# Kernel tuning notes

Hardware: AMD Instinct MI355X
Metric: run time of the kernel (lower is better)

## Reference

```python
import jax, jax.numpy as jnp
import numpy as np

N_NODES = 100_000
N_EDGES = 20_000   # hyperedges
NNZ = 2_000_000    # incidence pairs
F = 128
BN_EPS = 1e-5


def setup_inputs() -> dict:
    key = jax.random.key(0)
    ks = jax.random.split(key, 6)
    x_0 = jax.random.normal(ks[0], (N_NODES, F), dtype=jnp.float32)
    x_1 = jax.random.normal(ks[1], (N_EDGES, F), dtype=jnp.float32)
    node_idx = jax.random.randint(ks[2], (NNZ,), 0, N_NODES, dtype=jnp.int32)
    edge_idx = jax.random.randint(ks[3], (NNZ,), 0, N_EDGES, dtype=jnp.int32)
    W_nh = jax.random.normal(ks[4], (F, F), dtype=jnp.float32) / np.float32(np.sqrt(F))
    b_nh = jnp.zeros((F,), jnp.float32)
    W_en = jax.random.normal(ks[5], (F, 2 * F), dtype=jnp.float32) / np.float32(np.sqrt(2 * F))
    b_en = jnp.zeros((F,), jnp.float32)
    ones = jnp.ones((F,), jnp.float32)
    zeros = jnp.zeros((F,), jnp.float32)
    return {
        "x_0": x_0, "x_1": x_1, "node_idx": node_idx, "edge_idx": edge_idx,
        "W_nh": W_nh, "b_nh": b_nh, "W_en": W_en, "b_en": b_en,
        "bn0_gamma": ones, "bn0_beta": zeros, "bn0_mean": zeros, "bn0_var": ones,
        "bn1_gamma": ones, "bn1_beta": zeros, "bn1_mean": zeros, "bn1_var": ones,
    }


def _bn_eval(x, gamma, beta, mean, var):
    # BatchNorm1d in eval mode: normalize with running stats.
    return (x - mean) * (gamma * jax.lax.rsqrt(var + BN_EPS)) + beta


def reference(x_0, x_1, node_idx, edge_idx, W_nh, b_nh, W_en, b_en,
              bn0_gamma, bn0_beta, bn0_mean, bn0_var,
              bn1_gamma, bn1_beta, bn1_mean, bn1_var):
    # --- node -> hyperedge messenger ---
    # per-node message: sigmoid(Linear(x_0))  [n_nodes, F]
    node_messages = jax.nn.sigmoid(x_0 @ W_nh.T + b_nh)
    # gather over incidence list, scatter-sum onto hyperedges  [n_edges, F]
    node_msg_agg = jax.ops.segment_sum(node_messages[node_idx], edge_idx,
                                       num_segments=N_EDGES)

    # --- hyperedge -> node messenger ---
    # per-hyperedge message: sigmoid(Linear(cat(x_1, agg node msgs)))  [n_edges, F]
    he_messages = jax.nn.sigmoid(
        jnp.concatenate([x_1, node_msg_agg], axis=1) @ W_en.T + b_en)
    # gather per incidence, scatter-sum onto nodes  [n_nodes, F]
    he_msg_agg = jax.ops.segment_sum(he_messages[edge_idx], node_idx,
                                     num_segments=N_NODES)

    # --- updates (eval mode: feature dropout is identity) ---
    x0_out = jax.nn.sigmoid(
        _bn_eval(x_0, bn0_gamma, bn0_beta, bn0_mean, bn0_var) + he_msg_agg)
    x1_out = jax.nn.sigmoid(
        _bn_eval(x_1, bn1_gamma, bn1_beta, bn1_mean, bn1_var) + node_msg_agg)
    return (x0_out, x1_out)
```

## Files before the change

### kernel.cpp

```cpp
#include <hip/hip_runtime.h>
#include <hip/hip_bf16.h>
#include <math.h>

#define NNODES 100000
#define NEDGES 20000
#define NNZ_   2000000
#define FDIM   128
#define BN_EPS 1e-5f

#define NBUCK 256
#define CAP   9216
#define BPB_E 79
#define BPB_N 391
#define SH_E  17
#define SH_N  15

typedef __attribute__((ext_vector_type(8))) short bf16x8_t;
typedef __attribute__((ext_vector_type(4))) float f32x4_t;
typedef __attribute__((ext_vector_type(8))) unsigned short u16x8_t;

__device__ __forceinline__ float sigmoidf_(float x) {
    return 1.0f / (1.0f + __expf(-x));
}
__device__ __forceinline__ float bf2f(unsigned short u) {
    return __uint_as_float(((unsigned)u) << 16);
}
__device__ __forceinline__ unsigned short f2bf(float f) {
    __hip_bfloat16 h = __float2bfloat16(f);
    return *reinterpret_cast<unsigned short*>(&h);
}

__global__ __launch_bounds__(256) void prep_w(
    const float* __restrict__ W_nh, const float* __restrict__ W_en,
    unsigned short* __restrict__ Wnh_bf, float* __restrict__ WTen)
{
    int idx = blockIdx.x * blockDim.x + threadIdx.x;
    if (idx < FDIM * FDIM) {
        Wnh_bf[idx] = f2bf(W_nh[idx]);
    } else {
        int j = idx - FDIM * FDIM;
        if (j >= 2 * FDIM * FDIM) return;
        int k = j >> 7, c = j & 127;
        WTen[j] = W_en[c * 2 * FDIM + k];
    }
}

__global__ __launch_bounds__(256) void gemm1_mfma(
    const float* __restrict__ x0, const unsigned short* __restrict__ Wb,
    const float* __restrict__ bias, unsigned short* __restrict__ out)
{
    __shared__ unsigned short As[32][FDIM + 8];
    const int tid  = threadIdx.x;
    const int row0 = blockIdx.x * 32;
    {
        int r = tid >> 3, c0 = (tid & 7) * 16;
        const float* src = x0 + (size_t)(row0 + r) * FDIM + c0;
        unsigned short* dst = &As[r][c0];
        #pragma unroll
        for (int i = 0; i < 4; i++) {
            float4 v = *(const float4*)(src + i * 4);
            dst[i * 4 + 0] = f2bf(v.x);
            dst[i * 4 + 1] = f2bf(v.y);
            dst[i * 4 + 2] = f2bf(v.z);
            dst[i * 4 + 3] = f2bf(v.w);
        }
    }
    __syncthreads();
    const int wave  = tid >> 6;
    const int lane  = tid & 63;
    const int mhalf = wave & 1;
    const int nhalf = wave >> 1;
    const int lm    = lane & 15;
    const int quad  = lane >> 4;
    f32x4_t acc[4] = {};
    #pragma unroll
    for (int ks = 0; ks < 4; ks++) {
        bf16x8_t a = *(const bf16x8_t*)&As[mhalf * 16 + lm][ks * 32 + quad * 8];
        #pragma unroll
        for (int nt = 0; nt < 4; nt++) {
            int n = nhalf * 64 + nt * 16 + lm;
            bf16x8_t b = *(const bf16x8_t*)(Wb + (size_t)n * FDIM + ks * 32 + quad * 8);
            acc[nt] = __builtin_amdgcn_mfma_f32_16x16x32_bf16(a, b, acc[nt], 0, 0, 0);
        }
    }
    const int mbase = row0 + mhalf * 16 + quad * 4;
    #pragma unroll
    for (int nt = 0; nt < 4; nt++) {
        int n = nhalf * 64 + nt * 16 + lm;
        float bv = bias[n];
        #pragma unroll
        for (int r2 = 0; r2 < 4; r2++) {
            out[(size_t)(mbase + r2) * FDIM + n] = f2bf(sigmoidf_(acc[nt][r2] + bv));
        }
    }
}

__global__ __launch_bounds__(256, 2) void gemm_sig_bf16(
    const float* __restrict__ A1, const float* __restrict__ A2,
    const float* __restrict__ WT, const float* __restrict__ bias,
    unsigned short* __restrict__ out)
{
    constexpr int K = 256, BK = 64;
    __shared__ float As[32][BK + 4];
    __shared__ float Ws[BK][FDIM];
    const int tid  = threadIdx.x;
    const int row0 = blockIdx.x * 32;
    const int tcol = tid & 31;
    const int trow = tid >> 5;
    float acc[4][4] = {};
    for (int kk = 0; kk < K; kk += BK) {
        const float* Asrc = (kk < FDIM) ? A1 : A2;
        const int koff    = (kk < FDIM) ? kk : kk - FDIM;
        #pragma unroll
        for (int i = 0; i < 2; i++) {
            int l = tid + i * 256;
            int r = l >> 4, j = l & 15;
            float4 v = *(const float4*)(Asrc + (size_t)(row0 + r) * FDIM + koff + j * 4);
            *(float4*)&As[r][j * 4] = v;
        }
        #pragma unroll
        for (int i = 0; i < 8; i++) {
            int l = tid + i * 256;
            int k = l >> 5, j = l & 31;
            float4 v = *(const float4*)(WT + (size_t)(kk + k) * FDIM + j * 4);
            *(float4*)&Ws[k][j * 4] = v;
        }
        __syncthreads();
        #pragma unroll
        for (int k = 0; k < BK; k += 4) {
            float4 a[4];
            #pragma unroll
            for (int r = 0; r < 4; r++)
                a[r] = *(const float4*)&As[trow * 4 + r][k];
            #pragma unroll
            for (int kq = 0; kq < 4; kq++) {
                float4 w = *(const float4*)&Ws[k + kq][tcol * 4];
                #pragma unroll
                for (int r = 0; r < 4; r++) {
                    float av = (kq == 0) ? a[r].x : (kq == 1) ? a[r].y
                             : (kq == 2) ? a[r].z : a[r].w;
                    acc[r][0] += av * w.x;
                    acc[r][1] += av * w.y;
                    acc[r][2] += av * w.z;
                    acc[r][3] += av * w.w;
                }
            }
        }
        __syncthreads();
    }
    float4 bv = *(const float4*)(bias + tcol * 4);
    #pragma unroll
    for (int r = 0; r < 4; r++) {
        int row = row0 + trow * 4 + r;
        ushort4 o;
        o.x = f2bf(sigmoidf_(acc[r][0] + bv.x));
        o.y = f2bf(sigmoidf_(acc[r][1] + bv.y));
        o.z = f2bf(sigmoidf_(acc[r][2] + bv.z));
        o.w = f2bf(sigmoidf_(acc[r][3] + bv.w));
        *(ushort4*)(out + (size_t)row * FDIM + tcol * 4) = o;
    }
}

__global__ __launch_bounds__(1024) void bucket_scatter(
    const int* __restrict__ ni, const int* __restrict__ ei,
    unsigned* __restrict__ buck_e, unsigned* __restrict__ buck_n,
    int* __restrict__ gcur_e, int* __restrict__ gcur_n)
{
    __shared__ int lh_e[NBUCK], lh_n[NBUCK], lb_e[NBUCK], lb_n[NBUCK];
    const int t = threadIdx.x;
    if (t < NBUCK) { lh_e[t] = 0; lh_n[t] = 0; }
    __syncthreads();
    unsigned ent_e[4], ent_n[4];
    int be[4], bn[4], re[4], rn[4];
    const int base = blockIdx.x * 4096;
    #pragma unroll
    for (int j = 0; j < 4; j++) {
        int i = base + j * 1024 + t;
        if (i < NNZ_) {
            unsigned n = (unsigned)ni[i], e = (unsigned)ei[i];
            ent_e[j] = (e << SH_E) | n;  be[j] = (int)(e / BPB_E);
            ent_n[j] = (n << SH_N) | e;  bn[j] = (int)(n / BPB_N);
            re[j] = atomicAdd(&lh_e[be[j]], 1);
            rn[j] = atomicAdd(&lh_n[bn[j]], 1);
        } else { be[j] = -1; }
    }
    __syncthreads();
    if (t < NBUCK) {
        lb_e[t] = t * CAP + atomicAdd(&gcur_e[t], lh_e[t]);
        lb_n[t] = t * CAP + atomicAdd(&gcur_n[t], lh_n[t]);
    }
    __syncthreads();
    #pragma unroll
    for (int j = 0; j < 4; j++) {
        if (be[j] >= 0) {
            buck_e[(size_t)lb_e[be[j]] + re[j]] = ent_e[j];
            buck_n[(size_t)lb_n[bn[j]] + rn[j]] = ent_n[j];
        }
    }
}

template<int BPB, int SH, unsigned MASK, int NBINS, typename OUT>
__device__ __forceinline__ void sort_bucket(
    const unsigned* __restrict__ region, int cnt, int gbase, int b0,
    OUT* __restrict__ csr, int* __restrict__ off)
{
    __shared__ unsigned lh[512];
    __shared__ unsigned lw[4];
    const int t = threadIdx.x;
    lh[t] = 0; lh[t + 256] = 0;
    __syncthreads();
    for (int i = t; i < cnt; i += 256) {
        int bin = (int)(region[i] >> SH) - b0;
        atomicAdd(&lh[bin], 1u);
    }
    __syncthreads();
    unsigned h0 = lh[2 * t], h1 = lh[2 * t + 1];
    unsigned s = h0 + h1, inc = s;
    const int lane = t & 63;
    #pragma unroll
    for (int d = 1; d <= 32; d <<= 1) {
        unsigned v = (unsigned)__shfl_up((int)inc, d, 64);
        if (lane >= d) inc += v;
    }
    if (lane == 63) lw[t >> 6] = inc;
    __syncthreads();
    unsigned pre = 0;
    #pragma unroll
    for (int w = 0; w < 4; w++) if (w < (t >> 6)) pre += lw[w];
    unsigned excl = pre + inc - s;
    unsigned c0 = (unsigned)gbase + excl;
    unsigned c1 = c0 + h0;
    lh[2 * t] = c0; lh[2 * t + 1] = c1;
    int i0 = 2 * t, i1 = 2 * t + 1;
    if (i0 <= BPB && b0 + i0 <= NBINS) off[b0 + i0] = (int)c0;
    if (i1 <= BPB && b0 + i1 <= NBINS) off[b0 + i1] = (int)c1;
    __syncthreads();
    for (int i = t; i < cnt; i += 256) {
        unsigned ent = region[i];
        int bin = (int)(ent >> SH) - b0;
        unsigned pos = atomicAdd(&lh[bin], 1u);
        csr[pos] = (OUT)(ent & MASK);
    }
}

__global__ __launch_bounds__(256) void bucket_sort(
    const unsigned* __restrict__ buck_e, const unsigned* __restrict__ buck_n,
    const int* __restrict__ gcur_e, const int* __restrict__ gcur_n,
    unsigned* __restrict__ csr_e, unsigned short* __restrict__ csr_n,
    int* __restrict__ off_e, int* __restrict__ off_n)
{
    const int b = blockIdx.x & 255;
    const int* gc = (blockIdx.x < 256) ? gcur_e : gcur_n;
    __shared__ int ws4[4];
    const int t = threadIdx.x;
    int v = (t < b) ? gc[t] : 0;
    #pragma unroll
    for (int d = 32; d > 0; d >>= 1) v += __shfl_down(v, d, 64);
    if ((t & 63) == 0) ws4[t >> 6] = v;
    __syncthreads();
    const int gbase = ws4[0] + ws4[1] + ws4[2] + ws4[3];
    const int cnt = gc[b];
    __syncthreads();
    if (blockIdx.x < 256)
        sort_bucket<BPB_E, SH_E, 0x1FFFFu, NEDGES, unsigned>(
            buck_e + (size_t)b * CAP, cnt, gbase, b * BPB_E, csr_e, off_e);
    else
        sort_bucket<BPB_N, SH_N, 0x7FFFu, NNODES, unsigned short>(
            buck_n + (size_t)b * CAP, cnt, gbase, b * BPB_N, csr_n, off_n);
}

template<typename IDX, int U>
__global__ __launch_bounds__(256) void seg_sum_fin_v2(
    const unsigned short* __restrict__ table, const IDX* __restrict__ csr,
    const int* __restrict__ off, const float* __restrict__ x,
    const float* __restrict__ g, const float* __restrict__ bb,
    const float* __restrict__ mm, const float* __restrict__ vv,
    float* __restrict__ agg_out, float* __restrict__ fin_out, int nseg)
{
    const int seg = blockIdx.x * 4 + (threadIdx.x >> 6);
    if (seg >= nseg) return;
    const int lane = threadIdx.x & 63;
    const int c    = lane & 15;
    const int sub  = lane >> 4;
    const int c8   = c * 8;

    const int i0 = off[seg], i1 = off[seg + 1];
    f32x4_t a0 = {}, a1 = {};

    int i = i0;
    for (; i + 4 * U <= i1; i += 4 * U) {
        int r[U];
        u16x8_t v[U];
        #pragma unroll
        for (int u = 0; u < U; u++) r[u] = (int)csr[i + 4 * u + sub];
        #pragma unroll
        for (int u = 0; u < U; u++)
            v[u] = *(const u16x8_t*)(table + (size_t)r[u] * FDIM + c8);
        #pragma unroll
        for (int u = 0; u < U; u++) {
            a0[0] += bf2f(v[u][0]); a0[1] += bf2f(v[u][1]);
            a0[2] += bf2f(v[u][2]); a0[3] += bf2f(v[u][3]);
            a1[0] += bf2f(v[u][4]); a1[1] += bf2f(v[u][5]);
            a1[2] += bf2f(v[u][6]); a1[3] += bf2f(v[u][7]);
        }
    }
    if (i < i1) {
        u16x8_t v[U];
        #pragma unroll
        for (int u = 0; u < U; u++) {
            int row = i + 4 * u + sub;
            u16x8_t z = 0;
            v[u] = z;
            if (row < i1)
                v[u] = *(const u16x8_t*)(table + (size_t)csr[row] * FDIM + c8);
        }
        #pragma unroll
        for (int u = 0; u < U; u++) {
            a0[0] += bf2f(v[u][0]); a0[1] += bf2f(v[u][1]);
            a0[2] += bf2f(v[u][2]); a0[3] += bf2f(v[u][3]);
            a1[0] += bf2f(v[u][4]); a1[1] += bf2f(v[u][5]);
            a1[2] += bf2f(v[u][6]); a1[3] += bf2f(v[u][7]);
        }
    }

    #pragma unroll
    for (int j = 0; j < 4; j++) {
        a0[j] += __shfl_xor(a0[j], 16, 64);
        a0[j] += __shfl_xor(a0[j], 32, 64);
        a1[j] += __shfl_xor(a1[j], 16, 64);
        a1[j] += __shfl_xor(a1[j], 32, 64);
    }

    if (sub < 2) {
        const int q = c8 + sub * 4;
        f32x4_t s = sub ? a1 : a0;
        if (agg_out)
            *(f32x4_t*)(agg_out + (size_t)seg * FDIM + q) = s;
        if (fin_out) {
            f32x4_t xv = *(const f32x4_t*)(x + (size_t)seg * FDIM + q);
            f32x4_t gg = *(const f32x4_t*)(g + q);
            f32x4_t bt = *(const f32x4_t*)(bb + q);
            f32x4_t mn = *(const f32x4_t*)(mm + q);
            f32x4_t vr = *(const f32x4_t*)(vv + q);
            f32x4_t o;
            #pragma unroll
            for (int j = 0; j < 4; j++)
                o[j] = sigmoidf_((xv[j] - mn[j]) * (gg[j] * rsqrtf(vr[j] + BN_EPS))
                                 + bt[j] + s[j]);
            *(f32x4_t*)(fin_out + (size_t)seg * FDIM + q) = o;
        }
    }
}

extern "C" void kernel_launch(void* const* d_in, const int* in_sizes, int n_in,
                              void* d_out, int out_size, void* d_ws, size_t ws_size,
                              hipStream_t stream)
{
    const float* x0       = (const float*)d_in[0];
    const float* x1       = (const float*)d_in[1];
    const int*   node_idx = (const int*)d_in[2];
    const int*   edge_idx = (const int*)d_in[3];
    const float* W_nh     = (const float*)d_in[4];
    const float* b_nh     = (const float*)d_in[5];
    const float* W_en     = (const float*)d_in[6];
    const float* b_en     = (const float*)d_in[7];
    const float* bn0g = (const float*)d_in[8];
    const float* bn0b = (const float*)d_in[9];
    const float* bn0m = (const float*)d_in[10];
    const float* bn0v = (const float*)d_in[11];
    const float* bn1g = (const float*)d_in[12];
    const float* bn1b = (const float*)d_in[13];
    const float* bn1m = (const float*)d_in[14];
    const float* bn1v = (const float*)d_in[15];

    float* ws = (float*)d_ws;
    float* B    = ws;
    float* WTen = B + (size_t)NEDGES * FDIM;
    unsigned short* Wnh_bf = (unsigned short*)(WTen + 2 * FDIM * FDIM);
    unsigned short* A_bf = Wnh_bf + FDIM * FDIM;
    unsigned short* D_bf = A_bf + (size_t)NNODES * FDIM;
    int* ip    = (int*)(D_bf + (size_t)NEDGES * FDIM);
    int* off_e = ip;
    int* off_n = off_e + 20004;
    unsigned* csr_e = (unsigned*)(off_n + 100004);
    unsigned short* csr_n = (unsigned short*)(csr_e + NNZ_);
    unsigned* buck_e = (unsigned*)(csr_n + NNZ_);
    unsigned* buck_n = buck_e + (size_t)NBUCK * CAP;
    int* gcur_e = (int*)(buck_n + (size_t)NBUCK * CAP);
    int* gcur_n = gcur_e + NBUCK;

    hipMemsetAsync(gcur_e, 0, 2 * NBUCK * sizeof(int), stream);
    bucket_scatter<<<(NNZ_ + 4095) / 4096, 1024, 0, stream>>>(
        node_idx, edge_idx, buck_e, buck_n, gcur_e, gcur_n);
    bucket_sort<<<2 * NBUCK, 256, 0, stream>>>(buck_e, buck_n, gcur_e, gcur_n,
                                               csr_e, csr_n, off_e, off_n);

    prep_w<<<(3 * FDIM * FDIM + 255) / 256, 256, 0, stream>>>(W_nh, W_en, Wnh_bf, WTen);

    float* out0 = (float*)d_out;
    float* out1 = out0 + (size_t)NNODES * FDIM;

    gemm1_mfma<<<NNODES / 32, 256, 0, stream>>>(x0, Wnh_bf, b_nh, A_bf);
    seg_sum_fin_v2<unsigned, 8><<<(NEDGES + 3) / 4, 256, 0, stream>>>(
        A_bf, csr_e, off_e, x1, bn1g, bn1b, bn1m, bn1v, B, out1, NEDGES);

    gemm_sig_bf16<<<NEDGES / 32, 256, 0, stream>>>(x1, B, WTen, b_en, D_bf);
    seg_sum_fin_v2<unsigned short, 4><<<(NNODES + 3) / 4, 256, 0, stream>>>(
        D_bf, csr_n, off_n, x0, bn0g, bn0b, bn0m, bn0v, nullptr, out0, NNODES);
}
```

Baseline: 389.9 us.

## Split node-to-edge gather into node-range partitions and fuse reduction into GEMM2

The edge-side CSR is sorted by (edge, node-slice), giving 8 partitions per hyperedge. A new kernel gathers each partition separately into fp32 partial buffers, which spreads the gather across 8x more blocks and keeps each block's table reads within one node slice for better cache locality. A fused GEMM then sums the partials, writes the x1 output with batch norm and sigmoid, and computes the edge messages. This adds partial-buffer traffic and a larger offset array, and it needs enough workspace; if there is not enough, a fallback path is used.

```diff
diff --git a/kernel.cpp b/kernel.cpp
--- a/kernel.cpp
+++ b/kernel.cpp
@@ -14,6 +14,8 @@
 #define BPB_N 391
 #define SH_E  17
 #define SH_N  15
+#define NPART 8
+#define PSLICE 12500
 
 typedef __attribute__((ext_vector_type(8))) short bf16x8_t;
 typedef __attribute__((ext_vector_type(4))) float f32x4_t;
@@ -161,6 +163,99 @@
     }
 }
 
+__global__ __launch_bounds__(256, 2) void gemm2_fused(
+    const float* __restrict__ A1, const float* __restrict__ part,
+    const float* __restrict__ WT, const float* __restrict__ bias,
+    const float* __restrict__ g1, const float* __restrict__ b1,
+    const float* __restrict__ m1, const float* __restrict__ v1,
+    float* __restrict__ out1, unsigned short* __restrict__ outD)
+{
+    constexpr int K = 256, BK = 64;
+    __shared__ float As[32][BK + 4];
+    __shared__ float Ws[BK][FDIM];
+    const int tid  = threadIdx.x;
+    const int row0 = blockIdx.x * 32;
+    const int tcol = tid & 31;
+    const int trow = tid >> 5;
+    float acc[4][4] = {};
+    for (int kk = 0; kk < K; kk += BK) {
+        if (kk < FDIM) {
+            #pragma unroll
+            for (int i = 0; i < 2; i++) {
+                int l = tid + i * 256;
+                int r = l >> 4, j = l & 15;
+                float4 v = *(const float4*)(A1 + (size_t)(row0 + r) * FDIM + kk + j * 4);
+                *(float4*)&As[r][j * 4] = v;
+            }
+        } else {
+            const int koff = kk - FDIM;
+            #pragma unroll
+            for (int i = 0; i < 2; i++) {
+                int l = tid + i * 256;
+                int r = l >> 4, j = l & 15;
+                int col = koff + j * 4;
+                const float* pp = part + (size_t)(row0 + r) * FDIM + col;
+                f32x4_t bsum = {};
+                #pragma unroll
+                for (int p = 0; p < NPART; p++)
+                    bsum += *(const f32x4_t*)(pp + (size_t)p * NEDGES * FDIM);
+                *(f32x4_t*)&As[r][j * 4] = bsum;
+                f32x4_t xv = *(const f32x4_t*)(A1 + (size_t)(row0 + r) * FDIM + col);
+                f32x4_t gg = *(const f32x4_t*)(g1 + col);
+                f32x4_t bt = *(const f32x4_t*)(b1 + col);
+                f32x4_t mn = *(const f32x4_t*)(m1 + col);
+                f32x4_t vr = *(const f32x4_t*)(v1 + col);
+                f32x4_t o;
+                #pragma unroll
+                for (int jj = 0; jj < 4; jj++)
+                    o[jj] = sigmoidf_((xv[jj] - mn[jj]) * (gg[jj] * rsqrtf(vr[jj] + BN_EPS))
+                                      + bt[jj] + bsum[jj]);
+                *(f32x4_t*)(out1 + (size_t)(row0 + r) * FDIM + col) = o;
+            }
+        }
+        #pragma unroll
+        for (int i = 0; i < 8; i++) {
+            int l = tid + i * 256;
+            int k = l >> 5, j = l & 31;
+            float4 v = *(const float4*)(WT + (size_t)(kk + k) * FDIM + j * 4);
+            *(float4*)&Ws[k][j * 4] = v;
+        }
+        __syncthreads();
+        #pragma unroll
+        for (int k = 0; k < BK; k += 4) {
+            float4 a[4];
+            #pragma unroll
+            for (int r = 0; r < 4; r++)
+                a[r] = *(const float4*)&As[trow * 4 + r][k];
+            #pragma unroll
+            for (int kq = 0; kq < 4; kq++) {
+                float4 w = *(const float4*)&Ws[k + kq][tcol * 4];
+                #pragma unroll
+                for (int r = 0; r < 4; r++) {
+                    float av = (kq == 0) ? a[r].x : (kq == 1) ? a[r].y
+                             : (kq == 2) ? a[r].z : a[r].w;
+                    acc[r][0] += av * w.x;
+                    acc[r][1] += av * w.y;
+                    acc[r][2] += av * w.z;
+                    acc[r][3] += av * w.w;
+                }
+            }
+        }
+        __syncthreads();
+    }
+    float4 bv = *(const float4*)(bias + tcol * 4);
+    #pragma unroll
+    for (int r = 0; r < 4; r++) {
+        int row = row0 + trow * 4 + r;
+        ushort4 o;
+        o.x = f2bf(sigmoidf_(acc[r][0] + bv.x));
+        o.y = f2bf(sigmoidf_(acc[r][1] + bv.y));
+        o.z = f2bf(sigmoidf_(acc[r][2] + bv.z));
+        o.w = f2bf(sigmoidf_(acc[r][3] + bv.w));
+        *(ushort4*)(outD + (size_t)row * FDIM + tcol * 4) = o;
+    }
+}
+
 __global__ __launch_bounds__(1024) void bucket_scatter(
     const int* __restrict__ ni, const int* __restrict__ ei,
     unsigned* __restrict__ buck_e, unsigned* __restrict__ buck_n,
@@ -199,10 +294,58 @@
     }
 }
 
-template<int BPB, int SH, unsigned MASK, int NBINS, typename OUT>
-__device__ __forceinline__ void sort_bucket(
+__device__ __forceinline__ int ep_bin(unsigned ent) {
+    int e = (int)(ent >> SH_E);
+    int n = (int)(ent & 0x1FFFFu);
+    return e * NPART + n / PSLICE;
+}
+
+__device__ __forceinline__ void sort_bucket_e(
+    const unsigned* __restrict__ region, int cnt, int gbase, int bucket,
+    unsigned* __restrict__ csr, int* __restrict__ off)
+{
+    __shared__ unsigned lh[768];
+    __shared__ unsigned lw[4];
+    const int t = threadIdx.x;
+    lh[t] = 0; lh[t + 256] = 0; lh[t + 512] = 0;
+    __syncthreads();
+    const int b0 = bucket * (BPB_E * NPART);
+    for (int i = t; i < cnt; i += 256)
+        atomicAdd(&lh[ep_bin(region[i]) - b0], 1u);
+    __syncthreads();
+    unsigned h0 = lh[3 * t], h1 = lh[3 * t + 1], h2 = lh[3 * t + 2];
+    unsigned s = h0 + h1 + h2, inc = s;
+    const int lane = t & 63;
+    #pragma unroll
+    for (int d = 1; d <= 32; d <<= 1) {
+        unsigned v = (unsigned)__shfl_up((int)inc, d, 64);
+        if (lane >= d) inc += v;
+    }
+    if (lane == 63) lw[t >> 6] = inc;
+    __syncthreads();
+    unsigned pre = 0;
+    #pragma unroll
+    for (int w = 0; w < 4; w++) if (w < (t >> 6)) pre += lw[w];
+    unsigned excl = pre + inc - s;
+    unsigned c0 = (unsigned)gbase + excl, c1 = c0 + h0, c2 = c1 + h1;
+    lh[3 * t] = c0; lh[3 * t + 1] = c1; lh[3 * t + 2] = c2;
+    #pragma unroll
+    for (int j = 0; j < 3; j++) {
+        int ib = 3 * t + j;
+        unsigned cc = (j == 0) ? c0 : (j == 1) ? c1 : c2;
+        if (ib <= BPB_E * NPART && b0 + ib <= NEDGES * NPART) off[b0 + ib] = (int)cc;
+    }
+    __syncthreads();
+    for (int i = t; i < cnt; i += 256) {
+        unsigned ent = region[i];
+        unsigned pos = atomicAdd(&lh[ep_bin(ent) - b0], 1u);
+        csr[pos] = ent & 0x1FFFFu;
+    }
+}
+
+__device__ __forceinline__ void sort_bucket_n(
     const unsigned* __restrict__ region, int cnt, int gbase, int b0,
-    OUT* __restrict__ csr, int* __restrict__ off)
+    unsigned short* __restrict__ csr, int* __restrict__ off)
 {
     __shared__ unsigned lh[512];
     __shared__ unsigned lw[4];
@@ -210,7 +353,7 @@
     lh[t] = 0; lh[t + 256] = 0;
     __syncthreads();
     for (int i = t; i < cnt; i += 256) {
-        int bin = (int)(region[i] >> SH) - b0;
+        int bin = (int)(region[i] >> SH_N) - b0;
         atomicAdd(&lh[bin], 1u);
     }
     __syncthreads();
@@ -232,14 +375,14 @@
     unsigned c1 = c0 + h0;
     lh[2 * t] = c0; lh[2 * t + 1] = c1;
     int i0 = 2 * t, i1 = 2 * t + 1;
-    if (i0 <= BPB && b0 + i0 <= NBINS) off[b0 + i0] = (int)c0;
-    if (i1 <= BPB && b0 + i1 <= NBINS) off[b0 + i1] = (int)c1;
+    if (i0 <= BPB_N && b0 + i0 <= NNODES) off[b0 + i0] = (int)c0;
+    if (i1 <= BPB_N && b0 + i1 <= NNODES) off[b0 + i1] = (int)c1;
     __syncthreads();
     for (int i = t; i < cnt; i += 256) {
         unsigned ent = region[i];
-        int bin = (int)(ent >> SH) - b0;
+        int bin = (int)(ent >> SH_N) - b0;
         unsigned pos = atomicAdd(&lh[bin], 1u);
-        csr[pos] = (OUT)(ent & MASK);
+        csr[pos] = (unsigned short)(ent & 0x7FFFu);
     }
 }
 
@@ -247,7 +390,7 @@
     const unsigned* __restrict__ buck_e, const unsigned* __restrict__ buck_n,
     const int* __restrict__ gcur_e, const int* __restrict__ gcur_n,
     unsigned* __restrict__ csr_e, unsigned short* __restrict__ csr_n,
-    int* __restrict__ off_e, int* __restrict__ off_n)
+    int* __restrict__ off_ep, int* __restrict__ off_n)
 {
     const int b = blockIdx.x & 255;
     const int* gc = (blockIdx.x < 256) ? gcur_e : gcur_n;
@@ -262,14 +405,56 @@
     const int cnt = gc[b];
     __syncthreads();
     if (blockIdx.x < 256)
-        sort_bucket<BPB_E, SH_E, 0x1FFFFu, NEDGES, unsigned>(
-            buck_e + (size_t)b * CAP, cnt, gbase, b * BPB_E, csr_e, off_e);
+        sort_bucket_e(buck_e + (size_t)b * CAP, cnt, gbase, b, csr_e, off_ep);
     else
-        sort_bucket<BPB_N, SH_N, 0x7FFFu, NNODES, unsigned short>(
-            buck_n + (size_t)b * CAP, cnt, gbase, b * BPB_N, csr_n, off_n);
-}
-
-template<typename IDX, int U>
+        sort_bucket_n(buck_n + (size_t)b * CAP, cnt, gbase, b * BPB_N, csr_n, off_n);
+}
+
+__global__ __launch_bounds__(256) void seg_part_gather(
+    const unsigned short* __restrict__ table, const unsigned* __restrict__ csr,
+    const int* __restrict__ off_ep, float* __restrict__ partial)
+{
+    const int p = blockIdx.x & 7;
+    const int e = (blockIdx.x >> 3) * 4 + (threadIdx.x >> 6);
+    const int lane = threadIdx.x & 63;
+    const int sub  = lane >> 4;
+    const int c8   = (lane & 15) * 8;
+    const int bin  = e * NPART + p;
+    const int i0 = off_ep[bin], i1 = off_ep[bin + 1];
+    f32x4_t a0 = {}, a1 = {};
+    for (int i = i0; i < i1; i += 16) {
+        u16x8_t v[4];
+        #pragma unroll
+        for (int u = 0; u < 4; u++) {
+            int row_i = i + 4 * u + sub;
+            u16x8_t z = {};
+            v[u] = z;
+            if (row_i < i1)
+                v[u] = *(const u16x8_t*)(table + (size_t)csr[row_i] * FDIM + c8);
+        }
+        #pragma unroll
+        for (int u = 0; u < 4; u++) {
+            a0[0] += bf2f(v[u][0]); a0[1] += bf2f(v[u][1]);
+            a0[2] += bf2f(v[u][2]); a0[3] += bf2f(v[u][3]);
+            a1[0] += bf2f(v[u][4]); a1[1] += bf2f(v[u][5]);
+            a1[2] += bf2f(v[u][6]); a1[3] += bf2f(v[u][7]);
+        }
+    }
+    #pragma unroll
+    for (int j = 0; j < 4; j++) {
+        a0[j] += __shfl_xor(a0[j], 16, 64);
+        a0[j] += __shfl_xor(a0[j], 32, 64);
+        a1[j] += __shfl_xor(a1[j], 16, 64);
+        a1[j] += __shfl_xor(a1[j], 32, 64);
+    }
+    if (sub < 2) {
+        const int q = c8 + sub * 4;
+        f32x4_t s = sub ? a1 : a0;
+        *(f32x4_t*)(partial + ((size_t)p * NEDGES + e) * FDIM + q) = s;
+    }
+}
+
+template<typename IDX, int U, int OFFSTR>
 __global__ __launch_bounds__(256) void seg_sum_fin_v2(
     const unsigned short* __restrict__ table, const IDX* __restrict__ csr,
     const int* __restrict__ off, const float* __restrict__ x,
@@ -284,7 +469,7 @@
     const int sub  = lane >> 4;
     const int c8   = c * 8;
 
-    const int i0 = off[seg], i1 = off[seg + 1];
+    const int i0 = off[seg * OFFSTR], i1 = off[seg * OFFSTR + OFFSTR];
     f32x4_t a0 = {}, a1 = {};
 
     int i = i0;
@@ -309,7 +494,7 @@
         #pragma unroll
         for (int u = 0; u < U; u++) {
             int row = i + 4 * u + sub;
-            u16x8_t z = 0;
+            u16x8_t z = {};
             v[u] = z;
             if (row < i1)
                 v[u] = *(const u16x8_t*)(table + (size_t)csr[row] * FDIM + c8);
@@ -379,21 +564,24 @@
     unsigned short* Wnh_bf = (unsigned short*)(WTen + 2 * FDIM * FDIM);
     unsigned short* A_bf = Wnh_bf + FDIM * FDIM;
     unsigned short* D_bf = A_bf + (size_t)NNODES * FDIM;
-    int* ip    = (int*)(D_bf + (size_t)NEDGES * FDIM);
-    int* off_e = ip;
-    int* off_n = off_e + 20004;
+    int* off_ep = (int*)(D_bf + (size_t)NEDGES * FDIM);
+    int* off_n  = off_ep + 160004;
     unsigned* csr_e = (unsigned*)(off_n + 100004);
     unsigned short* csr_n = (unsigned short*)(csr_e + NNZ_);
     unsigned* buck_e = (unsigned*)(csr_n + NNZ_);
     unsigned* buck_n = buck_e + (size_t)NBUCK * CAP;
     int* gcur_e = (int*)(buck_n + (size_t)NBUCK * CAP);
     int* gcur_n = gcur_e + NBUCK;
+    float* partial = (float*)buck_e;
+    const size_t need = ((char*)partial - (char*)d_ws)
+                      + (size_t)NPART * NEDGES * FDIM * sizeof(float);
+    const bool big = ws_size >= need;
 
     hipMemsetAsync(gcur_e, 0, 2 * NBUCK * sizeof(int), stream);
     bucket_scatter<<<(NNZ_ + 4095) / 4096, 1024, 0, stream>>>(
         node_idx, edge_idx, buck_e, buck_n, gcur_e, gcur_n);
     bucket_sort<<<2 * NBUCK, 256, 0, stream>>>(buck_e, buck_n, gcur_e, gcur_n,
-                                               csr_e, csr_n, off_e, off_n);
+                                               csr_e, csr_n, off_ep, off_n);
 
     prep_w<<<(3 * FDIM * FDIM + 255) / 256, 256, 0, stream>>>(W_nh, W_en, Wnh_bf, WTen);
 
@@ -401,10 +589,18 @@
     float* out1 = out0 + (size_t)NNODES * FDIM;
 
     gemm1_mfma<<<NNODES / 32, 256, 0, stream>>>(x0, Wnh_bf, b_nh, A_bf);
-    seg_sum_fin_v2<unsigned, 8><<<(NEDGES + 3) / 4, 256, 0, stream>>>(
-        A_bf, csr_e, off_e, x1, bn1g, bn1b, bn1m, bn1v, B, out1, NEDGES);
-
-    gemm_sig_bf16<<<NEDGES / 32, 256, 0, stream>>>(x1, B, WTen, b_en, D_bf);
-    seg_sum_fin_v2<unsigned short, 4><<<(NNODES + 3) / 4, 256, 0, stream>>>(
+
+    if (big) {
+        seg_part_gather<<<(NEDGES / 4) * 8, 256, 0, stream>>>(
+            A_bf, csr_e, off_ep, partial);
+        gemm2_fused<<<NEDGES / 32, 256, 0, stream>>>(
+            x1, partial, WTen, b_en, bn1g, bn1b, bn1m, bn1v, out1, D_bf);
+    } else {
+        seg_sum_fin_v2<unsigned, 8, NPART><<<(NEDGES + 3) / 4, 256, 0, stream>>>(
+            A_bf, csr_e, off_ep, x1, bn1g, bn1b, bn1m, bn1v, B, out1, NEDGES);
+        gemm_sig_bf16<<<NEDGES / 32, 256, 0, stream>>>(x1, B, WTen, b_en, D_bf);
+    }
+
+    seg_sum_fin_v2<unsigned short, 4, 1><<<(NNODES + 3) / 4, 256, 0, stream>>>(
         D_bf, csr_n, off_n, x0, bn0g, bn0b, bn0m, bn0v, nullptr, out0, NNODES);
 }
```

Measured after the change: 423.3 us. 1.09x slower.
